# Optimization experiments

Hardware: AMD Instinct MI355X
Metric: run time of the kernel (lower is better)

The kernel has to match this reference:

```python
import jax, jax.numpy as jnp
import numpy as np

TOP_K = 2


def setup_inputs() -> dict:
    key = jax.random.key(0)
    k0, k1, k2, k3, k4 = jax.random.split(key, 5)
    B, S, D, F, E = 4, 2048, 2048, 1408, 8
    scale = 0.02
    return {
        "hidden_states": jax.random.normal(k0, (B, S, D), jnp.float32),
        "router_w": jax.random.normal(k1, (D, E), jnp.float32) * scale,
        "w_gate": jax.random.normal(k2, (E, D, F), jnp.float32) * scale,
        "w_up": jax.random.normal(k3, (E, D, F), jnp.float32) * scale,
        "w_down": jax.random.normal(k4, (E, F, D), jnp.float32) * scale,
    }


def reference(hidden_states, router_w, w_gate, w_up, w_down):
    B, S, D = hidden_states.shape
    x = hidden_states.reshape(-1, D)              # [N, D]
    N = x.shape[0]
    E = router_w.shape[-1]

    # ---- Router: softmax over experts, top-k, renormalize top-k probs ----
    logits = x @ router_w                         # [N, E]
    probs = jax.nn.softmax(logits, axis=-1)
    top_w, top_i = jax.lax.top_k(probs, TOP_K)    # [N, K]
    top_w = top_w / jnp.sum(top_w, axis=-1, keepdims=True)

    # Dense gate matrix [N, E]: gate is the (renormalized) routing weight for
    # selected experts, zero otherwise.
    gates = jnp.zeros_like(probs).at[jnp.arange(N)[:, None], top_i].set(top_w)

    # ---- Load-balancing aux loss (Switch-style, averaged over top-k) ----
    f = jnp.mean(jnp.sum(jax.nn.one_hot(top_i, E, dtype=x.dtype), axis=1), axis=0)  # [E] dispatch fraction
    P = jnp.mean(probs, axis=0)                   # [E] mean router prob
    aux_loss = (E / TOP_K) * jnp.sum(f * P)

    # ---- Per-expert SwiGLU FFN, computed as grouped GEMMs over all experts ----
    g = jnp.einsum("nd,edf->enf", x, w_gate)      # [E, N, F]
    u = jnp.einsum("nd,edf->enf", x, w_up)        # [E, N, F]
    h = jax.nn.silu(g) * u                        # [E, N, F]
    expert_out = jnp.einsum("enf,efd->end", h, w_down)  # [E, N, D]

    # ---- Combine: gate-weighted sum over experts ----
    out = jnp.einsum("ne,end->nd", gates, expert_out)   # [N, D]
    return out.reshape(B, S, D), aux_loss
```

## Files before the change

kernel.cpp:

```cpp
#include <hip/hip_runtime.h>

#define N_TOK 8192
#define DIM   2048
#define FFN   1408

#define XB_OFF  0ull
#define HP_OFF  0ull
#define XGP_OFF 49020928ull
#define EO_OFF  49020928ull
#define P1_OFF  120324096ull
#define P2_OFF  212598784ull
#define LPK_OFF 258736128ull
#define TI_OFF  258801664ull
#define TW_OFF  258834432ull
#define TP_OFF  258867200ull
#define ST_OFF  258932736ull

typedef __bf16 bf16x8 __attribute__((ext_vector_type(8)));
typedef float  f32x4  __attribute__((ext_vector_type(4)));
typedef int    int4v  __attribute__((ext_vector_type(4)));
typedef __attribute__((address_space(1))) void as1_void;
typedef __attribute__((address_space(3))) void as3_void;

__device__ __forceinline__ void gload16(const void* g, void* l) {
  __builtin_amdgcn_global_load_lds((as1_void*)g, (as3_void*)l, 16, 0, 0);
}

__device__ __forceinline__ ushort f2bf(float f) {
  unsigned u = __builtin_bit_cast(unsigned, f);
  u += 0x7FFFu + ((u >> 16) & 1u);
  return (ushort)(u >> 16);
}
__device__ __forceinline__ float blo(unsigned w) { return __builtin_bit_cast(float, w << 16); }
__device__ __forceinline__ float bhi(unsigned w) { return __builtin_bit_cast(float, w & 0xffff0000u); }

__device__ __forceinline__ int4v dsread(int addr) {
  int4v d;
  asm volatile("ds_read_b128 %0, %1" : "=v"(d) : "v"(addr));
  return d;
}

#define BAR()   __builtin_amdgcn_s_barrier()
#define MFMA16(a, b, c) __builtin_amdgcn_mfma_f32_16x16x32_bf16(a, b, c, 0, 0, 0)
#define BC(x) __builtin_bit_cast(bf16x8, x)

__device__ __forceinline__ int swz(int row, int s) {
  int q = row >> 1;
  int p = (((row & 1) << 2) | s) ^ (q & 7);
  return q * 128 + p * 16;
}

__global__ __launch_bounds__(256) void prep_kernel(
    const float* __restrict__ x, const float* __restrict__ rw,
    ushort* __restrict__ xb, int* __restrict__ topi, float* __restrict__ topw,
    int* __restrict__ cnt, unsigned long long* __restrict__ psum,
    const float* __restrict__ wg, const float* __restrict__ wu,
    const float* __restrict__ wd, char* __restrict__ p1, char* __restrict__ p2)
{
  __shared__ char smem[16640];
  int b = blockIdx.x;

  if (b < 512) {
    int tid = threadIdx.x, lane = tid & 63, wv = tid >> 6;
    float (*sP)[8] = (float(*)[8])smem;
    int   (*sC)[8] = (int(*)[8])(smem + 128);
    float pacc[8]; int cacc[8];
    #pragma unroll
    for (int e = 0; e < 8; ++e) { pacc[e] = 0.f; cacc[e] = 0; }

    #pragma unroll 1
    for (int it = 0; it < 4; ++it) {
      int t = b * 16 + wv * 4 + it;
      const float4* xr = (const float4*)(x + (size_t)t * DIM);
      float acc[8];
      #pragma unroll
      for (int e = 0; e < 8; ++e) acc[e] = 0.f;
      #pragma unroll 1
      for (int i = 0; i < 8; ++i) {
        int j = i * 64 + lane;
        float4 v = xr[j];
        ushort4 o; o.x = f2bf(v.x); o.y = f2bf(v.y); o.z = f2bf(v.z); o.w = f2bf(v.w);
        *(ushort4*)(xb + (size_t)t * DIM + (size_t)j * 4) = o;
        const float* rr = rw + (size_t)j * 32;
        #pragma unroll
        for (int c = 0; c < 4; ++c) {
          float xv = (&v.x)[c];
          const float4* r4 = (const float4*)(rr + c * 8);
          float4 q0 = r4[0], q1 = r4[1];
          acc[0] += xv * q0.x; acc[1] += xv * q0.y; acc[2] += xv * q0.z; acc[3] += xv * q0.w;
          acc[4] += xv * q1.x; acc[5] += xv * q1.y; acc[6] += xv * q1.z; acc[7] += xv * q1.w;
        }
      }
      #pragma unroll
      for (int off = 32; off; off >>= 1) {
        #pragma unroll
        for (int e = 0; e < 8; ++e) acc[e] += __shfl_xor(acc[e], off);
      }
      float m = acc[0];
      #pragma unroll
      for (int e = 1; e < 8; ++e) m = fmaxf(m, acc[e]);
      float p[8], s = 0.f;
      #pragma unroll
      for (int e = 0; e < 8; ++e) { p[e] = __expf(acc[e] - m); s += p[e]; }
      float inv = 1.f / s;
      int i1 = 0; float p1v = p[0];
      #pragma unroll
      for (int e = 1; e < 8; ++e) if (p[e] > p1v) { p1v = p[e]; i1 = e; }
      int i2 = -1; float p2v = -1.f;
      #pragma unroll
      for (int e = 0; e < 8; ++e) if (e != i1 && p[e] > p2v) { p2v = p[e]; i2 = e; }
      float w1 = p1v / (p1v + p2v);
      if (lane == 0) {
        topi[t] = i1 | (i2 << 8);
        topw[t] = w1;
        #pragma unroll
        for (int e = 0; e < 8; ++e) pacc[e] += p[e] * inv;
        cacc[i1]++; cacc[i2]++;
      }
    }
    if (lane == 0) {
      #pragma unroll
      for (int e = 0; e < 8; ++e) { sP[wv][e] = pacc[e]; sC[wv][e] = cacc[e]; }
    }
    __syncthreads();
    if (tid < 8) {
      float ps = sP[0][tid] + sP[1][tid] + sP[2][tid] + sP[3][tid];
      int   cs = sC[0][tid] + sC[1][tid] + sC[2][tid] + sC[3][tid];
      atomicAdd(&cnt[tid], cs);
      atomicAdd(&psum[tid], (unsigned long long)((double)ps * 1099511627776.0));
    }
  } else if (b < 11776) {
    int q_ = b - 512;
    int j = q_ & 63, rest = q_ >> 6;
    int tn = rest % 22, e = rest / 22;
    float (*tg)[65] = (float(*)[65])smem;
    float (*tu)[65] = (float(*)[65])(smem + 8320);
    int t = threadIdx.x;
    const float* gs = wg + ((size_t)e * DIM + j * 32) * FFN + tn * 64;
    const float* us = wu + ((size_t)e * DIM + j * 32) * FFN + tn * 64;
    #pragma unroll
    for (int k2 = 0; k2 < 2; ++k2) {
      int idx = t + k2 * 256;
      int kk = idx >> 4, fq = idx & 15;
      *(float4*)&tg[kk][fq * 4] = *(const float4*)(gs + (size_t)kk * FFN + fq * 4);
      *(float4*)&tu[kk][fq * 4] = *(const float4*)(us + (size_t)kk * FFN + fq * 4);
    }
    __syncthreads();
    char* dst = p1 + ((size_t)((e * 22 + tn) * 64 + j)) * 8192;
    #pragma unroll
    for (int k2 = 0; k2 < 2; ++k2) {
      int L = t + k2 * 256;
      int q = L >> 3, v = (L & 7) ^ (q & 7);
      int r = 2 * q + (v >> 2), s = v & 3;
      const float* col = (r < 64) ? &tg[s * 8][r] : &tu[s * 8][r - 64];
      ushort u8[8];
      #pragma unroll
      for (int i = 0; i < 8; ++i) u8[i] = f2bf(col[i * 65]);
      *(ushort4*)(dst + (size_t)L * 16) = *(ushort4*)&u8[0];
      *(ushort4*)(dst + (size_t)L * 16 + 8) = *(ushort4*)&u8[4];
    }
  } else {
    int q_ = b - 11776;
    int j = q_ % 44, rest = q_ / 44;
    int tn = rest & 15, e = rest >> 4;
    float (*t2)[129] = (float(*)[129])smem;
    int t = threadIdx.x;
    const float* src = wd + ((size_t)e * FFN + j * 32) * DIM + tn * 128;
    #pragma unroll
    for (int k2 = 0; k2 < 4; ++k2) {
      int idx = t + k2 * 256;
      int kk = idx >> 5, dq = idx & 31;
      *(float4*)&t2[kk][dq * 4] = *(const float4*)(src + (size_t)kk * DIM + dq * 4);
    }
    __syncthreads();
    char* dst = p2 + ((size_t)((e * 16 + tn) * 44 + j)) * 8192;
    #pragma unroll
    for (int k2 = 0; k2 < 2; ++k2) {
      int L = t + k2 * 256;
      int q = L >> 3, v = (L & 7) ^ (q & 7);
      int r = 2 * q + (v >> 2), s = v & 3;
      ushort u8[8];
      #pragma unroll
      for (int i = 0; i < 8; ++i) u8[i] = f2bf(t2[s * 8 + i][r]);
      *(ushort4*)(dst + (size_t)L * 16) = *(ushort4*)&u8[0];
      *(ushort4*)(dst + (size_t)L * 16 + 8) = *(ushort4*)&u8[4];
    }
  }
}

__global__ void scan_aux_kernel(int* __restrict__ stats,
                                const unsigned long long* __restrict__ psum,
                                float* __restrict__ aux_out)
{
  if (threadIdx.x == 0 && blockIdx.x == 0) {
    int b = 0, tb = 0;
    for (int e = 0; e < 8; ++e) {
      stats[8 + e] = b; stats[16 + e] = b; stats[24 + e] = tb;
      tb += (stats[e] + 127) >> 7;
      b += stats[e];
    }
    stats[32] = tb;
    double s = 0.0;
    for (int e = 0; e < 8; ++e)
      s += (double)stats[e] * ((double)psum[e] * (1.0 / 1099511627776.0));
    aux_out[0] = (float)(4.0 * s / ((double)N_TOK * (double)N_TOK));
  }
}

__global__ __launch_bounds__(256) void place_kernel(
    const int* __restrict__ topi, int* __restrict__ stats,
    int* __restrict__ lpk, int2* __restrict__ tpos)
{
  int t = blockIdx.x * 256 + threadIdx.x;
  if (t >= N_TOK) return;
  int pk = topi[t];
  int e1 = pk & 0xff, e2 = (pk >> 8) & 0xff;
  int p1 = atomicAdd(&stats[8 + e1], 1);
  lpk[p1] = t;
  int p2 = atomicAdd(&stats[8 + e2], 1);
  lpk[p2] = t;
  tpos[t] = make_int2(p1, p2);
}

__global__ __launch_bounds__(256) void gather_x_kernel(
    const ushort* __restrict__ xb, const int* __restrict__ lpk,
    const int* __restrict__ stats, char* __restrict__ xgp)
{
  int b = blockIdx.x;
  int tile = b >> 1;
  if (tile >= stats[32]) return;
  int e = 0;
  #pragma unroll
  for (int k = 1; k < 8; ++k) if (tile >= stats[24 + k]) e = k;
  int tloc = tile - stats[24 + e];
  int abase = stats[16 + e], Me = stats[e];
  int half = b & 1;
  int lane = threadIdx.x & 63, wv = threadIdx.x >> 6;
  char* base = xgp + (size_t)tile * 64 * 8192;
  #pragma unroll 1
  for (int r = half * 64 + wv; r < half * 64 + 64; r += 4) {
    int lrow = tloc * 128 + r;
    bool valid = lrow < Me;
    const char* src = (const char*)xb + (valid ? (size_t)lpk[abase + lrow] * (DIM * 2) : 0);
    int q = r >> 1;
    #pragma unroll
    for (int it = 0; it < 4; ++it) {
      int c16 = it * 64 + lane;
      int j = c16 >> 2, s = c16 & 3;
      uint4 v;
      if (valid) v = *(const uint4*)(src + c16 * 16);
      else       v = make_uint4(0, 0, 0, 0);
      int p = (((r & 1) << 2) | s) ^ (q & 7);
      *(uint4*)(base + (size_t)j * 8192 + q * 128 + p * 16) = v;
    }
  }
}


#define GSTAGE(J, BUF) do { \
  size_t go_ = (size_t)(J) * 8192 + wv * 2048 + lane * 16; \
  int d_ = (BUF) * 24576 + wv * 2048; \
  gload16(aP0 + go_,        sm + d_); \
  gload16(aP0 + go_ + 1024, sm + d_ + 1024); \
  gload16(aP1 + go_,        sm + d_ + 8192); \
  gload16(aP1 + go_ + 1024, sm + d_ + 8192 + 1024); \
  gload16(bP + go_,         sm + d_ + 16384); \
  gload16(bP + go_ + 1024,  sm + d_ + 16384 + 1024); \
} while (0)

#define KLOOP(NCH) \
  GSTAGE(0, 0); \
  _Pragma("unroll 1") \
  for (int j = 0; j < (NCH); ++j) { \
    if (j + 1 < (NCH)) { \
      GSTAGE(j + 1, (j + 1) & 1); \
      asm volatile("s_waitcnt vmcnt(6)" ::: "memory"); \
    } else { \
      asm volatile("s_waitcnt vmcnt(0)" ::: "memory"); \
    } \
    BAR(); \
    int sb = (j & 1) * 24576; \
    int4v va[4], vb[8]; \
    _Pragma("unroll") for (int n = 0; n < 4; ++n) vb[n] = dsread(sb + adB[n]); \
    _Pragma("unroll") for (int m = 0; m < 4; ++m) va[m] = dsread(sb + adA[m]); \
    _Pragma("unroll") for (int n = 4; n < 8; ++n) vb[n] = dsread(sb + adB[n]); \
    asm volatile("s_waitcnt lgkmcnt(4)" ::: "memory"); \
    __builtin_amdgcn_sched_barrier(0); \
    __builtin_amdgcn_s_setprio(1); \
    _Pragma("unroll") for (int m = 0; m < 4; ++m) \
      _Pragma("unroll") for (int n = 0; n < 4; ++n) \
        acc[m][n] = MFMA16(BC(va[m]), BC(vb[n]), acc[m][n]); \
    __builtin_amdgcn_s_setprio(0); \
    asm volatile("s_waitcnt lgkmcnt(0)" ::: "memory"); \
    __builtin_amdgcn_sched_barrier(0); \
    __builtin_amdgcn_s_setprio(1); \
    _Pragma("unroll") for (int m = 0; m < 4; ++m) \
      _Pragma("unroll") for (int n = 4; n < 8; ++n) \
        acc[m][n] = MFMA16(BC(va[m]), BC(vb[n]), acc[m][n]); \
    __builtin_amdgcn_s_setprio(0); \
    BAR(); \
  }

__global__ __launch_bounds__(256, 2) void gemm_gu_kernel(
    const char* __restrict__ xgp, const char* __restrict__ p1,
    const int* __restrict__ stats, char* __restrict__ hp)
{
  int bid = blockIdx.x;
  int e = bid & 7;
  int Ll = bid >> 3;
  int tm = Ll / 22, tn = Ll % 22;
  int Me = stats[e];
  if (tm * 256 >= Me) return;
  int tb = stats[24 + e];

  __shared__ char sm[49152];
  int tid = threadIdx.x, lane = tid & 63, wv = tid >> 6;
  const char* aP0 = xgp + (size_t)(tb + tm * 2) * 64 * 8192;
  const char* aP1 = aP0 + 64 * 8192;
  const char* bP = p1 + (size_t)((e * 22 + tn) * 64) * 8192;

  int s = lane >> 4;
  int adA[4], adB[8];
  #pragma unroll
  for (int m = 0; m < 4; ++m) {
    int row = wv * 64 + m * 16 + (lane & 15);
    adA[m] = (row >> 7) * 8192 + swz(row & 127, s);
  }
  #pragma unroll
  for (int n = 0; n < 8; ++n) adB[n] = 16384 + swz(n * 16 + (lane & 15), s);

  f32x4 acc[4][8];
  #pragma unroll
  for (int m = 0; m < 4; ++m)
    #pragma unroll
    for (int n = 0; n < 8; ++n) acc[m][n] = (f32x4){0, 0, 0, 0};

  KLOOP(64);

  int r0 = (lane >> 4) * 4, cl = lane & 15;
  #pragma unroll
  for (int m = 0; m < 4; ++m) {
    #pragma unroll
    for (int r = 0; r < 4; ++r) {
      int row = wv * 64 + m * 16 + r0 + r;
      if (tm * 256 + row < Me) {
        char* hb = hp + (size_t)(tb + tm * 2 + (row >> 7)) * 44 * 8192;
        int lr = row & 127;
        int q = lr >> 1;
        #pragma unroll
        for (int n = 0; n < 4; ++n) {
          float g = acc[m][n][r];
          float u = acc[m][n + 4][r];
          float hv = g * u / (1.f + __expf(-g));
          int f = tn * 64 + n * 16 + cl;
          int j2 = f >> 5, s2 = (f >> 3) & 3, i2 = f & 7;
          int p = (((lr & 1) << 2) | s2) ^ (q & 7);
          *(ushort*)(hb + (size_t)j2 * 8192 + q * 128 + p * 16 + i2 * 2) = f2bf(hv);
        }
      }
    }
  }
}

__global__ __launch_bounds__(256, 2) void gemm_down_kernel(
    const char* __restrict__ hp, const char* __restrict__ p2,
    const int* __restrict__ stats, ushort* __restrict__ eo)
{
  int bid = blockIdx.x;
  int e = bid & 7;
  int Ll = bid >> 3;
  int tm = Ll >> 4, tn = Ll & 15;
  int Me = stats[e];
  if (tm * 256 >= Me) return;
  int tb = stats[24 + e], abase = stats[16 + e];

  __shared__ char sm[49152];
  int tid = threadIdx.x, lane = tid & 63, wv = tid >> 6;
  const char* aP0 = hp + (size_t)(tb + tm * 2) * 44 * 8192;
  const char* aP1 = aP0 + 44 * 8192;
  const char* bP = p2 + (size_t)((e * 16 + tn) * 44) * 8192;

  int s = lane >> 4;
  int adA[4], adB[8];
  #pragma unroll
  for (int m = 0; m < 4; ++m) {
    int row = wv * 64 + m * 16 + (lane & 15);
    adA[m] = (row >> 7) * 8192 + swz(row & 127, s);
  }
  #pragma unroll
  for (int n = 0; n < 8; ++n) adB[n] = 16384 + swz(n * 16 + (lane & 15), s);

  f32x4 acc[4][8];
  #pragma unroll
  for (int m = 0; m < 4; ++m)
    #pragma unroll
    for (int n = 0; n < 8; ++n) acc[m][n] = (f32x4){0, 0, 0, 0};

  KLOOP(44);

  int c0 = lane & 15, r0 = (lane >> 4) * 4;
  #pragma unroll
  for (int m = 0; m < 4; ++m) {
    #pragma unroll
    for (int r = 0; r < 4; ++r) {
      int lrow = tm * 256 + wv * 64 + m * 16 + r0 + r;
      if (lrow < Me) {
        ushort* dst = eo + (size_t)(abase + lrow) * DIM + tn * 128 + c0;
        #pragma unroll
        for (int n = 0; n < 8; ++n) dst[n * 16] = f2bf(acc[m][n][r]);
      }
    }
  }
}

__global__ __launch_bounds__(256) void combine_kernel(
    const ushort* __restrict__ eo, const int2* __restrict__ tpos,
    const float* __restrict__ topw, float* __restrict__ out)
{
  int t = blockIdx.x;
  int2 tp = tpos[t];
  float w1 = topw[t], w2 = 1.f - w1;
  const uint4* r1 = (const uint4*)(eo + (size_t)tp.x * DIM);
  const uint4* r2 = (const uint4*)(eo + (size_t)tp.y * DIM);
  float4* o = (float4*)(out + (size_t)t * DIM);
  int i = threadIdx.x;
  uint4 a = r1[i], b = r2[i];
  float4 c0, c1;
  c0.x = w1 * blo(a.x) + w2 * blo(b.x);  c0.y = w1 * bhi(a.x) + w2 * bhi(b.x);
  c0.z = w1 * blo(a.y) + w2 * blo(b.y);  c0.w = w1 * bhi(a.y) + w2 * bhi(b.y);
  c1.x = w1 * blo(a.z) + w2 * blo(b.z);  c1.y = w1 * bhi(a.z) + w2 * bhi(b.z);
  c1.z = w1 * blo(a.w) + w2 * blo(b.w);  c1.w = w1 * bhi(a.w) + w2 * bhi(b.w);
  o[i * 2] = c0;
  o[i * 2 + 1] = c1;
}

extern "C" void kernel_launch(void* const* d_in, const int* in_sizes, int n_in,
                              void* d_out, int out_size, void* d_ws, size_t ws_size,
                              hipStream_t stream)
{
  const float* x  = (const float*)d_in[0];
  const float* rw = (const float*)d_in[1];
  const float* wg = (const float*)d_in[2];
  const float* wu = (const float*)d_in[3];
  const float* wd = (const float*)d_in[4];
  float* out = (float*)d_out;

  char* ws = (char*)d_ws;
  ushort* xb   = (ushort*)(ws + XB_OFF);
  char*   hp   = ws + HP_OFF;
  char*   xgp  = ws + XGP_OFF;
  ushort* eo   = (ushort*)(ws + EO_OFF);
  char*   p1   = ws + P1_OFF;
  char*   p2   = ws + P2_OFF;
  int*    lpk  = (int*)(ws + LPK_OFF);
  int*    topi = (int*)(ws + TI_OFF);
  float*  topw = (float*)(ws + TW_OFF);
  int2*   tpos = (int2*)(ws + TP_OFF);
  int*    stats = (int*)(ws + ST_OFF);
  unsigned long long* psum = (unsigned long long*)(ws + ST_OFF + 192);

  hipMemsetAsync(ws + ST_OFF, 0, 256, stream);

  prep_kernel<<<17408, 256, 0, stream>>>(x, rw, xb, topi, topw, stats, psum,
                                         wg, wu, wd, p1, p2);
  scan_aux_kernel<<<1, 64, 0, stream>>>(stats, psum, out + (size_t)out_size - 1);
  place_kernel<<<32, 256, 0, stream>>>(topi, stats, lpk, tpos);

  gather_x_kernel<<<272, 256, 0, stream>>>(xb, lpk, stats, xgp);

  gemm_gu_kernel<<<2816, 256, 0, stream>>>(xgp, p1, stats, hp);
  gemm_down_kernel<<<2048, 256, 0, stream>>>(hp, p2, stats, eo);

  combine_kernel<<<8192, 256, 0, stream>>>(eo, tpos, topw, out);
}
```

Baseline: 531.1 us.

## Triple-buffer GEMM K-loop, fuse scan into place kernel, split gather finer

The GEMM K-loops move from double to triple buffering, staging two chunks ahead with a deeper vmcnt wait, to hide more global-load latency. Shared memory per block grows from 48KB to 72KB, which with two blocks per CU may cut occupancy. The single-thread scan/aux kernel is folded into place_kernel: every block recomputes the prefix sums locally, removing one launch. The gather kernel now uses four blocks per tile instead of two to add parallelism.

```diff
diff --git a/kernel.cpp b/kernel.cpp
--- a/kernel.cpp
+++ b/kernel.cpp
@@ -188,36 +188,37 @@
   }
 }
 
-__global__ void scan_aux_kernel(int* __restrict__ stats,
-                                const unsigned long long* __restrict__ psum,
-                                float* __restrict__ aux_out)
-{
-  if (threadIdx.x == 0 && blockIdx.x == 0) {
-    int b = 0, tb = 0;
+__global__ __launch_bounds__(256) void place_kernel(
+    const int* __restrict__ topi, int* __restrict__ stats,
+    const unsigned long long* __restrict__ psum,
+    int* __restrict__ lpk, int2* __restrict__ tpos, float* __restrict__ aux_out)
+{
+  int cnt[8], pre[8];
+  int acc = 0;
+  #pragma unroll
+  for (int e = 0; e < 8; ++e) { cnt[e] = stats[e]; pre[e] = acc; acc += cnt[e]; }
+
+  if (blockIdx.x == 0 && threadIdx.x == 0) {
+    int tb = 0;
     for (int e = 0; e < 8; ++e) {
-      stats[8 + e] = b; stats[16 + e] = b; stats[24 + e] = tb;
-      tb += (stats[e] + 127) >> 7;
-      b += stats[e];
+      stats[16 + e] = pre[e];
+      stats[24 + e] = tb;
+      tb += (cnt[e] + 127) >> 7;
     }
     stats[32] = tb;
     double s = 0.0;
     for (int e = 0; e < 8; ++e)
-      s += (double)stats[e] * ((double)psum[e] * (1.0 / 1099511627776.0));
+      s += (double)cnt[e] * ((double)psum[e] * (1.0 / 1099511627776.0));
     aux_out[0] = (float)(4.0 * s / ((double)N_TOK * (double)N_TOK));
   }
-}
-
-__global__ __launch_bounds__(256) void place_kernel(
-    const int* __restrict__ topi, int* __restrict__ stats,
-    int* __restrict__ lpk, int2* __restrict__ tpos)
-{
+
   int t = blockIdx.x * 256 + threadIdx.x;
   if (t >= N_TOK) return;
   int pk = topi[t];
   int e1 = pk & 0xff, e2 = (pk >> 8) & 0xff;
-  int p1 = atomicAdd(&stats[8 + e1], 1);
+  int p1 = pre[e1] + atomicAdd(&stats[8 + e1], 1);
   lpk[p1] = t;
-  int p2 = atomicAdd(&stats[8 + e2], 1);
+  int p2 = pre[e2] + atomicAdd(&stats[8 + e2], 1);
   lpk[p2] = t;
   tpos[t] = make_int2(p1, p2);
 }
@@ -227,18 +228,18 @@
     const int* __restrict__ stats, char* __restrict__ xgp)
 {
   int b = blockIdx.x;
-  int tile = b >> 1;
+  int tile = b >> 2;
   if (tile >= stats[32]) return;
   int e = 0;
   #pragma unroll
   for (int k = 1; k < 8; ++k) if (tile >= stats[24 + k]) e = k;
   int tloc = tile - stats[24 + e];
   int abase = stats[16 + e], Me = stats[e];
-  int half = b & 1;
+  int quad = b & 3;
   int lane = threadIdx.x & 63, wv = threadIdx.x >> 6;
   char* base = xgp + (size_t)tile * 64 * 8192;
   #pragma unroll 1
-  for (int r = half * 64 + wv; r < half * 64 + 64; r += 4) {
+  for (int r = quad * 32 + wv; r < quad * 32 + 32; r += 4) {
     int lrow = tloc * 128 + r;
     bool valid = lrow < Me;
     const char* src = (const char*)xb + (valid ? (size_t)lpk[abase + lrow] * (DIM * 2) : 0);
@@ -270,16 +271,20 @@
 
 #define KLOOP(NCH) \
   GSTAGE(0, 0); \
+  GSTAGE(1, 1); \
+  { int cur = 0, st = 2; \
   _Pragma("unroll 1") \
   for (int j = 0; j < (NCH); ++j) { \
-    if (j + 1 < (NCH)) { \
-      GSTAGE(j + 1, (j + 1) & 1); \
+    if (j + 2 < (NCH)) { \
+      GSTAGE(j + 2, st); \
+      asm volatile("s_waitcnt vmcnt(12)" ::: "memory"); \
+    } else if (j + 2 == (NCH)) { \
       asm volatile("s_waitcnt vmcnt(6)" ::: "memory"); \
     } else { \
       asm volatile("s_waitcnt vmcnt(0)" ::: "memory"); \
     } \
     BAR(); \
-    int sb = (j & 1) * 24576; \
+    int sb = cur * 24576; \
     int4v va[4], vb[8]; \
     _Pragma("unroll") for (int n = 0; n < 4; ++n) vb[n] = dsread(sb + adB[n]); \
     _Pragma("unroll") for (int m = 0; m < 4; ++m) va[m] = dsread(sb + adA[m]); \
@@ -299,7 +304,9 @@
         acc[m][n] = MFMA16(BC(va[m]), BC(vb[n]), acc[m][n]); \
     __builtin_amdgcn_s_setprio(0); \
     BAR(); \
-  }
+    cur = (cur == 2) ? 0 : cur + 1; \
+    st  = (st  == 2) ? 0 : st  + 1; \
+  } }
 
 __global__ __launch_bounds__(256, 2) void gemm_gu_kernel(
     const char* __restrict__ xgp, const char* __restrict__ p1,
@@ -313,7 +320,7 @@
   if (tm * 256 >= Me) return;
   int tb = stats[24 + e];
 
-  __shared__ char sm[49152];
+  __shared__ char sm[73728];
   int tid = threadIdx.x, lane = tid & 63, wv = tid >> 6;
   const char* aP0 = xgp + (size_t)(tb + tm * 2) * 64 * 8192;
   const char* aP1 = aP0 + 64 * 8192;
@@ -374,7 +381,7 @@
   if (tm * 256 >= Me) return;
   int tb = stats[24 + e], abase = stats[16 + e];
 
-  __shared__ char sm[49152];
+  __shared__ char sm[73728];
   int tid = threadIdx.x, lane = tid & 63, wv = tid >> 6;
   const char* aP0 = hp + (size_t)(tb + tm * 2) * 44 * 8192;
   const char* aP1 = aP0 + 44 * 8192;
@@ -463,10 +470,10 @@
 
   prep_kernel<<<17408, 256, 0, stream>>>(x, rw, xb, topi, topw, stats, psum,
                                          wg, wu, wd, p1, p2);
-  scan_aux_kernel<<<1, 64, 0, stream>>>(stats, psum, out + (size_t)out_size - 1);
-  place_kernel<<<32, 256, 0, stream>>>(topi, stats, lpk, tpos);
-
-  gather_x_kernel<<<272, 256, 0, stream>>>(xb, lpk, stats, xgp);
+  place_kernel<<<32, 256, 0, stream>>>(topi, stats, psum, lpk, tpos,
+                                       out + (size_t)out_size - 1);
+
+  gather_x_kernel<<<544, 256, 0, stream>>>(xb, lpk, stats, xgp);
 
   gemm_gu_kernel<<<2816, 256, 0, stream>>>(xgp, p1, stats, hp);
   gemm_down_kernel<<<2048, 256, 0, stream>>>(hp, p2, stats, eo);
```

Result: faster. 517.4 us (median of 2 runs) (-2.6%).
